# Kernel optimization log

Measured on AMD Instinct MI355X. Metric: run time of the kernel, lower is better.

## Reference

```python
import jax, jax.numpy as jnp
import numpy as np

B, N, DIM = 1, 1024, 512
H, DH = 8, 64
TOPK_RATIO = 0.1
SCALE = DH ** -0.5
PH = 32  # phase MLP hidden = hidden_dim//2 = 64//2
INIT_SCALE = 0.02


def cayley(Mre, Mim):
    # CayleyLinear: unitary weight W = (I - A)^{-1} (I + A), A skew-Hermitian
    M = (Mre + 1j * Mim).astype(jnp.complex64) * INIT_SCALE
    A = M - M.conj().T
    I = jnp.eye(M.shape[0], dtype=M.dtype)
    return jnp.linalg.solve(I - A, I + A)


def phase_fn(mag, pw1, pb1, pw2, pb2):
    # PhaseModulation: MLP(|alpha|) + 0.1*|alpha| residual
    h = jax.nn.silu(mag[..., None] @ pw1 + pb1)  # (...,PH)
    out = (h @ pw2 + pb2)[..., 0]
    return out + mag * 0.1


def setup_inputs() -> dict:
    key = jax.random.key(0)
    ks = jax.random.split(key, 12)
    d = {
        'x_real': jax.random.normal(ks[0], (B, N, DIM), dtype=jnp.float32),
        'x_imag': jax.random.normal(ks[1], (B, N, DIM), dtype=jnp.float32),
    }
    for i, n in enumerate(['Wq', 'Wk', 'Wv', 'Wo']):
        d[n + '_re'] = jax.random.normal(ks[2 + 2 * i], (DIM, DIM), dtype=jnp.float32)
        d[n + '_im'] = jax.random.normal(ks[3 + 2 * i], (DIM, DIM), dtype=jnp.float32)
    d['pw1'] = jax.random.normal(ks[10], (1, PH), dtype=jnp.float32) * 0.1
    d['pb1'] = jnp.zeros((PH,), dtype=jnp.float32)
    d['pw2'] = jax.random.normal(ks[11], (PH, 1), dtype=jnp.float32) * 0.1
    d['pb2'] = jnp.zeros((1,), dtype=jnp.float32)
    return d


def reference(x_real, x_imag, Wq_re, Wq_im, Wk_re, Wk_im, Wv_re, Wv_im,
              Wo_re, Wo_im, pw1, pb1, pw2, pb2):
    x = (x_real + 1j * x_imag).astype(jnp.complex64)  # (B,N,D)
    Q = x @ cayley(Wq_re, Wq_im)
    K = x @ cayley(Wk_re, Wk_im)
    V = x @ cayley(Wv_re, Wv_im)
    # (B,N,D) -> (B,H,N,DH)
    Q = Q.reshape(B, N, H, DH).transpose(0, 2, 1, 3)
    K = K.reshape(B, N, H, DH).transpose(0, 2, 1, 3)
    V = V.reshape(B, N, H, DH).transpose(0, 2, 1, 3)
    # complex inner products: conj(Q) . K
    alpha = jnp.einsum('bhnd,bhsd->bhns', Q.conj(), K) * SCALE  # (B,H,N,N) complex
    mag = jnp.abs(alpha)
    phase = phase_fn(jax.lax.stop_gradient(mag), pw1, pb1, pw2, pb2)
    beta = alpha * jnp.exp(1j * phase.astype(jnp.complex64))
    # Born-rule normalization: p = |beta|^2 / sum |beta|^2
    b2 = beta.real ** 2 + beta.imag ** 2
    probs = b2 / b2.sum(axis=-1, keepdims=True)  # (B,H,N,N) real
    # top-k interference routing
    k = max(1, int(TOPK_RATIO * N))
    tp, ti = jax.lax.top_k(probs, k)  # (B,H,N,k)
    tpn = tp / (tp.sum(axis=-1, keepdims=True) + 1e-8)
    w = jax.nn.softmax(tpn * k, axis=-1)  # complex_softmax on real input
    # gather V rows per (b,h): (N,DH)[(N,k)] -> (N,k,DH), no NxN expand
    gather = jax.vmap(jax.vmap(lambda v, i: v[i]))
    V_topk = gather(V, ti)  # (B,H,N,k,DH) complex
    out = (w[..., None] * V_topk).sum(axis=3)  # (B,H,N,DH)
    out = out.transpose(0, 2, 1, 3).reshape(B, N, DIM)
    out = out @ cayley(Wo_re, Wo_im)
    return out  # complex64 (B,N,DIM)
```

## Files before the change

kernel.cpp:

```cpp
#include <hip/hip_runtime.h>
#include <math.h>


#define PLANE   262144
#define CMAT    524288
#define PPLANE  524288
#define CPROJ   1048576
#define KTOP    102

#define R_FLOATS 12582912
#define POOL_FLOATS (4*CMAT + 8192 + R_FLOATS)
__device__ __attribute__((aligned(256))) float g_pool[POOL_FLOATS];

__launch_bounds__(256)
__global__ void cgemm_kernel(
    const float* __restrict__ Are, const float* __restrict__ Aim, int sA,
    const float* __restrict__ Bre, const float* __restrict__ Bim, int sB,
    const float* __restrict__ Dre, const float* __restrict__ Dim, int sD,
    float* __restrict__ Cre, float* __restrict__ Cim, int sC,
    int M, int N, int Kd, float dcoef, int use_d)
{
    __shared__ float As_re[16][34], As_im[16][34];
    __shared__ float Bs_re[16][68], Bs_im[16][68];
    const int b = blockIdx.z;
    Are += (size_t)b * sA; Aim += (size_t)b * sA;
    Bre += (size_t)b * sB; Bim += (size_t)b * sB;
    Dre += (size_t)b * sD; Dim += (size_t)b * sD;
    Cre += (size_t)b * sC; Cim += (size_t)b * sC;
    const int tid = threadIdx.x;
    const int bm = blockIdx.y * 32, bn = blockIdx.x * 64;
    const int tm = (tid >> 4) << 1;
    const int tn = (tid & 15) << 2;
    const int lmA = tid >> 3;
    const int lkA = (tid & 7) << 1;
    const int lkB = tid >> 4;
    const int lnB = (tid & 15) << 2;
    float cr[2][4] = {{0.f}}, ci[2][4] = {{0.f}};
    const float* pAre = Are + (size_t)(bm + lmA) * Kd + lkA;
    const float* pAim = Aim + (size_t)(bm + lmA) * Kd + lkA;
    const float* pBre = Bre + (size_t)lkB * N + bn + lnB;
    const float* pBim = Bim + (size_t)lkB * N + bn + lnB;
    for (int k0 = 0; k0 < Kd; k0 += 16) {
        const float2 ar = *(const float2*)(pAre + k0);
        const float2 ai = *(const float2*)(pAim + k0);
        const float4 br = *(const float4*)(pBre + (size_t)k0 * N);
        const float4 bi = *(const float4*)(pBim + (size_t)k0 * N);
        __syncthreads();
        As_re[lkA+0][lmA] = ar.x; As_re[lkA+1][lmA] = ar.y;
        As_im[lkA+0][lmA] = ai.x; As_im[lkA+1][lmA] = ai.y;
        *(float4*)&Bs_re[lkB][lnB] = br;
        *(float4*)&Bs_im[lkB][lnB] = bi;
        __syncthreads();
        #pragma unroll
        for (int k = 0; k < 16; ++k) {
            const float2 xr = *(const float2*)&As_re[k][tm];
            const float2 xi = *(const float2*)&As_im[k][tm];
            const float4 yr = *(const float4*)&Bs_re[k][tn];
            const float4 yi = *(const float4*)&Bs_im[k][tn];
            const float axr[2] = {xr.x, xr.y};
            const float axi[2] = {xi.x, xi.y};
            const float byr[4] = {yr.x, yr.y, yr.z, yr.w};
            const float byi[4] = {yi.x, yi.y, yi.z, yi.w};
            #pragma unroll
            for (int i = 0; i < 2; ++i) {
                #pragma unroll
                for (int j = 0; j < 4; ++j) {
                    cr[i][j] += axr[i]*byr[j] - axi[i]*byi[j];
                    ci[i][j] += axr[i]*byi[j] + axi[i]*byr[j];
                }
            }
        }
    }
    #pragma unroll
    for (int i = 0; i < 2; ++i) {
        const size_t idx = (size_t)(bm + tm + i) * N + bn + tn;
        float4 vr = make_float4(cr[i][0], cr[i][1], cr[i][2], cr[i][3]);
        float4 vi = make_float4(ci[i][0], ci[i][1], ci[i][2], ci[i][3]);
        if (use_d) {
            const float4 dr4 = *(const float4*)(Dre + idx);
            const float4 di4 = *(const float4*)(Dim + idx);
            vr.x = dcoef*dr4.x - vr.x; vr.y = dcoef*dr4.y - vr.y;
            vr.z = dcoef*dr4.z - vr.z; vr.w = dcoef*dr4.w - vr.w;
            vi.x = dcoef*di4.x - vi.x; vi.y = dcoef*di4.y - vi.y;
            vi.z = dcoef*di4.z - vi.z; vi.w = dcoef*di4.w - vi.w;
        }
        *(float4*)(Cre + idx) = vr;
        *(float4*)(Cim + idx) = vi;
    }
}

__launch_bounds__(256)
__global__ void build_A_kernel(const float* __restrict__ W0re, const float* __restrict__ W0im,
                               const float* __restrict__ W1re, const float* __restrict__ W1im,
                               const float* __restrict__ W2re, const float* __restrict__ W2im,
                               const float* __restrict__ W3re, const float* __restrict__ W3im,
                               int aoff)
{
    float* Aout = g_pool + aoff;
    const int w = blockIdx.y;
    const float* Mre; const float* Mim;
    if      (w == 0) { Mre = W0re; Mim = W0im; }
    else if (w == 1) { Mre = W1re; Mim = W1im; }
    else if (w == 2) { Mre = W2re; Mim = W2im; }
    else             { Mre = W3re; Mim = W3im; }
    const int idx = blockIdx.x * 256 + threadIdx.x;
    const int i = idx >> 9, j = idx & 511;
    float* Are = Aout + (size_t)w * CMAT;
    float* Aim = Are + PLANE;
    Are[idx] = 0.02f * (Mre[i*512 + j] - Mre[j*512 + i]);
    Aim[idx] = 0.02f * (Mim[i*512 + j] + Mim[j*512 + i]);
}

__launch_bounds__(256)
__global__ void x0_kernel(const float* __restrict__ S, float* __restrict__ X)
{
    const float bc = -1.0f/7.0f;
    const float diagc = 6.0f/7.0f + bc;
    const int w = blockIdx.y;
    const int idx = blockIdx.x * 256 + threadIdx.x;
    const int i = idx >> 9, j = idx & 511;
    const float* Sre = S + (size_t)w * CMAT;
    const float* Sim = Sre + PLANE;
    float* Xre = X + (size_t)w * CMAT;
    float* Xim = Xre + PLANE;
    const float diag = (i == j) ? diagc : 0.0f;
    Xre[idx] = diag - bc * Sre[idx];
    Xim[idx] = -bc * Sim[idx];
}

__launch_bounds__(256)
__global__ void buildP_kernel(const float* __restrict__ A, const float* __restrict__ S,
                              float* __restrict__ P)
{
    const int w = blockIdx.y;
    const int idx = blockIdx.x * 256 + threadIdx.x;
    const int i = idx >> 9, j = idx & 511;
    const float* Are = A + (size_t)w * CMAT; const float* Aim = Are + PLANE;
    const float* Sre = S + (size_t)w * CMAT; const float* Sim = Sre + PLANE;
    float* Pre = P + (size_t)w * CMAT; float* Pim = Pre + PLANE;
    const float d = (i == j) ? 1.0f : 0.0f;
    Pre[idx] = d + 2.0f * Are[idx] + Sre[idx];
    Pim[idx] = 2.0f * Aim[idx] + Sim[idx];
}

__launch_bounds__(256)
__global__ void zero_kernel(float* __restrict__ p, int n)
{
    const int i = blockIdx.x * 256 + threadIdx.x;
    if (i < n) p[i] = 0.f;
}

__launch_bounds__(256)
__global__ void scores_kernel(const float* __restrict__ Qre, const float* __restrict__ Qim,
                              const float* __restrict__ Kre, const float* __restrict__ Kim,
                              float* __restrict__ B2, float* __restrict__ RS)
{
    __shared__ float Qs_re[16][68], Qs_im[16][68], Ks_re[16][68], Ks_im[16][68];
    __shared__ float rs[64];
    const int h = blockIdx.z;
    const int bm = blockIdx.y * 64, bn = blockIdx.x * 64;
    const int tid = threadIdx.x;
    const int tm = (tid >> 4) << 2, tn = (tid & 15) << 2;
    const int lm = tid >> 2, lk = (tid & 3) << 2;
    float dr[4][4] = {{0.f}}, di[4][4] = {{0.f}};
    for (int k0 = 0; k0 < 64; k0 += 16) {
        const float4 qr = *(const float4*)(Qre + (size_t)(bm+lm)*512 + h*64 + k0 + lk);
        const float4 qi = *(const float4*)(Qim + (size_t)(bm+lm)*512 + h*64 + k0 + lk);
        const float4 kr = *(const float4*)(Kre + (size_t)(bn+lm)*512 + h*64 + k0 + lk);
        const float4 ki = *(const float4*)(Kim + (size_t)(bn+lm)*512 + h*64 + k0 + lk);
        __syncthreads();
        Qs_re[lk+0][lm]=qr.x; Qs_re[lk+1][lm]=qr.y; Qs_re[lk+2][lm]=qr.z; Qs_re[lk+3][lm]=qr.w;
        Qs_im[lk+0][lm]=qi.x; Qs_im[lk+1][lm]=qi.y; Qs_im[lk+2][lm]=qi.z; Qs_im[lk+3][lm]=qi.w;
        Ks_re[lk+0][lm]=kr.x; Ks_re[lk+1][lm]=kr.y; Ks_re[lk+2][lm]=kr.z; Ks_re[lk+3][lm]=kr.w;
        Ks_im[lk+0][lm]=ki.x; Ks_im[lk+1][lm]=ki.y; Ks_im[lk+2][lm]=ki.z; Ks_im[lk+3][lm]=ki.w;
        __syncthreads();
        #pragma unroll
        for (int k = 0; k < 16; ++k) {
            const float4 xr = *(const float4*)&Qs_re[k][tm];
            const float4 xi = *(const float4*)&Qs_im[k][tm];
            const float4 yr = *(const float4*)&Ks_re[k][tn];
            const float4 yi = *(const float4*)&Ks_im[k][tn];
            const float axr[4] = {xr.x, xr.y, xr.z, xr.w};
            const float axi[4] = {xi.x, xi.y, xi.z, xi.w};
            const float byr[4] = {yr.x, yr.y, yr.z, yr.w};
            const float byi[4] = {yi.x, yi.y, yi.z, yi.w};
            #pragma unroll
            for (int i = 0; i < 4; ++i) {
                #pragma unroll
                for (int j = 0; j < 4; ++j) {
                    dr[i][j] += axr[i]*byr[j] + axi[i]*byi[j];
                    di[i][j] += axr[i]*byi[j] - axi[i]*byr[j];
                }
            }
        }
    }
    if (tid < 64) rs[tid] = 0.f;
    __syncthreads();
    float rpart[4] = {0.f, 0.f, 0.f, 0.f};
    #pragma unroll
    for (int i = 0; i < 4; ++i) {
        #pragma unroll
        for (int j = 0; j < 4; ++j) {
            const float b2v = (dr[i][j]*dr[i][j] + di[i][j]*di[i][j]) * 0.015625f;
            B2[(size_t)h*1048576 + (size_t)(bm+tm+i)*1024 + (bn+tn+j)] = b2v;
            rpart[i] += b2v;
        }
    }
    #pragma unroll
    for (int i = 0; i < 4; ++i) atomicAdd(&rs[tm+i], rpart[i]);
    __syncthreads();
    if (tid < 64) atomicAdd(&RS[h*1024 + bm + tid], rs[tid]);
}

__launch_bounds__(256)
__global__ void select_kernel(const float* __restrict__ B2, const float* __restrict__ RS,
                              const float* __restrict__ Vre, const float* __restrict__ Vim,
                              float* __restrict__ AOre, float* __restrict__ AOim)
{
    __shared__ float sv[1024];
    __shared__ unsigned int hist[256];
    __shared__ int ssum[256];
    __shared__ unsigned int sc[4];
    __shared__ float sel_v[104];
    __shared__ int sel_i[104];
    __shared__ float sel_w[104];
    __shared__ float rbuf[256];
    const int bid = blockIdx.x;
    const int h = bid >> 10, n = bid & 1023;
    const int tid = threadIdx.x;
    const float* row = B2 + (size_t)h * 1048576 + (size_t)n * 1024;
    #pragma unroll
    for (int e = 0; e < 4; ++e) sv[tid + 256*e] = row[tid + 256*e];
    if (tid == 0) sc[2] = 0u;
    __syncthreads();

    unsigned prefix = 0u, pmask = 0u;
    int krem = KTOP;
    for (int pass = 0; pass < 4; ++pass) {
        const int shift = 24 - 8 * pass;
        hist[tid] = 0u;
        __syncthreads();
        #pragma unroll
        for (int e = 0; e < 4; ++e) {
            const unsigned u = __float_as_uint(sv[tid + 256*e]);
            if ((u & pmask) == prefix) atomicAdd(&hist[(u >> shift) & 255u], 1u);
        }
        __syncthreads();
        ssum[tid] = (int)hist[tid];
        __syncthreads();
        for (int off = 1; off < 256; off <<= 1) {
            const int add = (tid + off < 256) ? ssum[tid + off] : 0;
            __syncthreads();
            ssum[tid] += add;
            __syncthreads();
        }
        const int above = (tid < 255) ? ssum[tid + 1] : 0;
        if (ssum[tid] >= krem && above < krem) {
            sc[0] = (unsigned)tid;
            sc[1] = (unsigned)(krem - above);
        }
        __syncthreads();
        prefix |= sc[0] << shift;
        pmask |= 0xFFu << shift;
        krem = (int)sc[1];
        __syncthreads();
    }
    const unsigned T = prefix;
    const int m = krem;

    #pragma unroll
    for (int e = 0; e < 4; ++e) {
        const int i = tid + 256*e;
        const float v = sv[i];
        const unsigned u = __float_as_uint(v);
        bool sel = (u > T);
        if (!sel && u == T) {
            int rank = 0;
            for (int j = 0; j < i; ++j) rank += (__float_as_uint(sv[j]) == T) ? 1 : 0;
            sel = (rank < m);
        }
        if (sel) {
            const unsigned p = atomicAdd(&sc[2], 1u);
            if (p < 104u) { sel_v[p] = v; sel_i[p] = i; }
        }
    }
    __syncthreads();

    rbuf[tid] = (tid < KTOP) ? sel_v[tid] : 0.f;
    __syncthreads();
    for (int st = 128; st > 0; st >>= 1) { if (tid < st) rbuf[tid] += rbuf[tid + st]; __syncthreads(); }
    const float sumtop = rbuf[0];
    __syncthreads();
    rbuf[tid] = (tid < KTOP) ? sel_v[tid] : -1.f;
    __syncthreads();
    for (int st = 128; st > 0; st >>= 1) { if (tid < st) rbuf[tid] = fmaxf(rbuf[tid], rbuf[tid + st]); __syncthreads(); }
    const float vmax = rbuf[0];
    __syncthreads();

    const float S_row = RS[(h << 10) + n];
    const float denom = sumtop + 1e-8f * S_row;
    const float scl = (float)KTOP / denom;
    if (tid < KTOP) sel_w[tid] = expf(sel_v[tid] * scl - vmax * scl);
    __syncthreads();
    rbuf[tid] = (tid < KTOP) ? sel_w[tid] : 0.f;
    __syncthreads();
    for (int st = 128; st > 0; st >>= 1) { if (tid < st) rbuf[tid] += rbuf[tid + st]; __syncthreads(); }
    const float Z = rbuf[0];
    __syncthreads();

    if (tid < 128) {
        const int d = tid & 63;
        const int im = tid >> 6;
        const float* Vp = im ? Vim : Vre;
        const int base = h * 64 + d;
        float acc = 0.f;
        for (int j = 0; j < KTOP; ++j) acc += sel_w[j] * Vp[(size_t)sel_i[j] * 512 + base];
        acc /= Z;
        float* AOp = im ? AOim : AOre;
        AOp[(size_t)n * 512 + h * 64 + d] = acc;
    }
}

__launch_bounds__(256)
__global__ void copy_out_kernel(const float* __restrict__ Y,
                                float* __restrict__ out, int out_floats)
{
    const int i = blockIdx.x * 256 + threadIdx.x;
    if (i < out_floats && i < 2*PPLANE) out[i] = Y[i];
}

extern "C" void kernel_launch(void* const* d_in, const int* in_sizes, int n_in,
                              void* d_out, int out_size, void* d_ws, size_t ws_size,
                              hipStream_t stream)
{
    (void)in_sizes; (void)n_in; (void)d_ws; (void)ws_size;
    const float* x_re = (const float*)d_in[0];
    const float* x_im = (const float*)d_in[1];

    float* pool = nullptr;
    hipGetSymbolAddress((void**)&pool, HIP_SYMBOL(g_pool));

    float* Wall = pool;
    float* RSg  = Wall + 4*CMAT;
    float* R    = RSg + 8192;
    float* A  = R;
    float* S  = R + 4*CMAT;
    float* X  = R + 8*CMAT;
    float* X2 = R + 12*CMAT;
    float* T  = R + 16*CMAT;
    float* Q  = R;
    float* Kp = R + CPROJ;
    float* V  = R + 2*CPROJ;
    float* AO = R + 3*CPROJ;
    float* B2 = R + 4*CPROJ;

    const int aoff = (int)(A - pool);

    build_A_kernel<<<dim3(1024,4),256,0,stream>>>(
        (const float*)d_in[2],(const float*)d_in[3],(const float*)d_in[4],(const float*)d_in[5],
        (const float*)d_in[6],(const float*)d_in[7],(const float*)d_in[8],(const float*)d_in[9], aoff);
    cgemm_kernel<<<dim3(8,16,4),256,0,stream>>>(A,A+PLANE,CMAT, A,A+PLANE,CMAT,
                                                A,A+PLANE,CMAT, S,S+PLANE,CMAT,
                                                512,512,512, 0.f,0);
    x0_kernel<<<dim3(1024,4),256,0,stream>>>(S, X);
    float* Xc = X; float* Xn = X2;
    for (int it = 0; it < 4; ++it) {
        cgemm_kernel<<<dim3(8,16,4),256,0,stream>>>(S,S+PLANE,CMAT, Xc,Xc+PLANE,CMAT,
                                                    Xc,Xc+PLANE,CMAT, T,T+PLANE,CMAT,
                                                    512,512,512, 1.f,1);
        cgemm_kernel<<<dim3(8,16,4),256,0,stream>>>(Xc,Xc+PLANE,CMAT, T,T+PLANE,CMAT,
                                                    Xc,Xc+PLANE,CMAT, Xn,Xn+PLANE,CMAT,
                                                    512,512,512, 2.f,1);
        float* tmp = Xc; Xc = Xn; Xn = tmp;
    }
    buildP_kernel<<<dim3(1024,4),256,0,stream>>>(A, S, T);
    cgemm_kernel<<<dim3(8,16,4),256,0,stream>>>(T,T+PLANE,CMAT, Xc,Xc+PLANE,CMAT,
                                                T,T+PLANE,CMAT, Wall,Wall+PLANE,CMAT,
                                                512,512,512, 0.f,0);

    cgemm_kernel<<<dim3(8,32,3),256,0,stream>>>(x_re,x_im,0, Wall,Wall+PLANE,CMAT,
                                                x_re,x_im,0, Q,Q+PPLANE,CPROJ,
                                                1024,512,512, 0.f,0);

    zero_kernel<<<32,256,0,stream>>>(RSg, 8192);
    scores_kernel<<<dim3(16,16,8),256,0,stream>>>(Q,Q+PPLANE, Kp,Kp+PPLANE, B2, RSg);
    select_kernel<<<8192,256,0,stream>>>(B2, RSg, V,V+PPLANE, AO,AO+PPLANE);

    float* Y = B2;
    cgemm_kernel<<<dim3(8,32,1),256,0,stream>>>(AO,AO+PPLANE,0, Wall+3*CMAT,Wall+3*CMAT+PLANE,0,
                                                AO,AO+PPLANE,0, Y,Y+PPLANE,0,
                                                1024,512,512, 0.f,0);
    copy_out_kernel<<<4096,256,0,stream>>>(Y, (float*)d_out, out_size);
}
```

Baseline: 1.208 ms.

## Use degree-4 polynomial initial guess to halve Newton-Schulz iterations for Cayley inverse

```diff
diff --git a/kernel.cpp b/kernel.cpp
--- a/kernel.cpp
+++ b/kernel.cpp
@@ -112,20 +112,31 @@
 }
 
 __launch_bounds__(256)
-__global__ void x0_kernel(const float* __restrict__ S, float* __restrict__ X)
-{
-    const float bc = -1.0f/7.0f;
-    const float diagc = 6.0f/7.0f + bc;
+__global__ void u_kernel(const float* __restrict__ S, const float* __restrict__ S2,
+                         float* __restrict__ U)
+{
+    const int w = blockIdx.y;
+    const int idx = blockIdx.x * 256 + threadIdx.x;
+    const size_t off = (size_t)w * CMAT;
+    U[off + idx] = 5.5f * S[off + idx] + 0.5f * S2[off + idx];
+}
+
+__launch_bounds__(256)
+__global__ void x0deg4_kernel(const float* __restrict__ S, const float* __restrict__ S2,
+                              const float* __restrict__ V, float* __restrict__ X)
+{
+    const float inv = 1.0f/61.5f;
     const int w = blockIdx.y;
     const int idx = blockIdx.x * 256 + threadIdx.x;
     const int i = idx >> 9, j = idx & 511;
-    const float* Sre = S + (size_t)w * CMAT;
-    const float* Sim = Sre + PLANE;
-    float* Xre = X + (size_t)w * CMAT;
-    float* Xim = Xre + PLANE;
-    const float diag = (i == j) ? diagc : 0.0f;
-    Xre[idx] = diag - bc * Sre[idx];
-    Xim[idx] = -bc * Sim[idx];
+    const size_t off = (size_t)w * CMAT;
+    const float* Sre = S + off;   const float* Sim = Sre + PLANE;
+    const float* S2re = S2 + off; const float* S2im = S2re + PLANE;
+    const float* Vre = V + off;   const float* Vim = Vre + PLANE;
+    float* Xre = X + off; float* Xim = Xre + PLANE;
+    const float diag = (i == j) ? 60.5f : 0.0f;
+    Xre[idx] = (diag + 48.f * Sre[idx] + 23.f * S2re[idx] + Vre[idx]) * inv;
+    Xim[idx] = (       48.f * Sim[idx] + 23.f * S2im[idx] + Vim[idx]) * inv;
 }
 
 __launch_bounds__(256)
@@ -345,9 +356,10 @@
     float* R    = RSg + 8192;
     float* A  = R;
     float* S  = R + 4*CMAT;
-    float* X  = R + 8*CMAT;
-    float* X2 = R + 12*CMAT;
-    float* T  = R + 16*CMAT;
+    float* S2 = R + 8*CMAT;
+    float* X  = R + 12*CMAT;
+    float* X2 = R + 16*CMAT;
+    float* T  = R + 20*CMAT;
     float* Q  = R;
     float* Kp = R + CPROJ;
     float* V  = R + 2*CPROJ;
@@ -362,9 +374,16 @@
     cgemm_kernel<<<dim3(8,16,4),256,0,stream>>>(A,A+PLANE,CMAT, A,A+PLANE,CMAT,
                                                 A,A+PLANE,CMAT, S,S+PLANE,CMAT,
                                                 512,512,512, 0.f,0);
-    x0_kernel<<<dim3(1024,4),256,0,stream>>>(S, X);
+    cgemm_kernel<<<dim3(8,16,4),256,0,stream>>>(S,S+PLANE,CMAT, S,S+PLANE,CMAT,
+                                                S,S+PLANE,CMAT, S2,S2+PLANE,CMAT,
+                                                512,512,512, 0.f,0);
+    u_kernel<<<dim3(2048,4),256,0,stream>>>(S, S2, X);
+    cgemm_kernel<<<dim3(8,16,4),256,0,stream>>>(S2,S2+PLANE,CMAT, X,X+PLANE,CMAT,
+                                                S2,S2+PLANE,CMAT, X2,X2+PLANE,CMAT,
+                                                512,512,512, 0.f,0);
+    x0deg4_kernel<<<dim3(1024,4),256,0,stream>>>(S, S2, X2, X);
     float* Xc = X; float* Xn = X2;
-    for (int it = 0; it < 4; ++it) {
+    for (int it = 0; it < 2; ++it) {
         cgemm_kernel<<<dim3(8,16,4),256,0,stream>>>(S,S+PLANE,CMAT, Xc,Xc+PLANE,CMAT,
                                                     Xc,Xc+PLANE,CMAT, T,T+PLANE,CMAT,
                                                     512,512,512, 1.f,1);
```

Result: faster. 1.066 ms (-11.7%).
